# Kernel tuning notes

Hardware: AMD Instinct MI355X
Metric: run time of the kernel (lower is better)

## Reference

```python
import jax, jax.numpy as jnp
import numpy as np
import math

B, S, HID, H = 2, 4096, 512, 8
D_K = HID // H


def setup_inputs() -> dict:
    key = jax.random.key(0)
    ks = jax.random.split(key, 8)
    inp = {
        "query": jax.random.normal(ks[0], (B, S, HID), dtype=jnp.float32),
        "key": jax.random.normal(ks[1], (B, S, HID), dtype=jnp.float32),
        "value": jax.random.normal(ks[2], (B, S, HID), dtype=jnp.float32),
        "mask": jax.random.randint(ks[3], (B, S), 0, 2, dtype=jnp.int32),
        # conv1d kernel_size=1, bias=False -> plain [out,in] weights (xavier-normal-ish)
        "Wq": jax.random.normal(ks[4], (HID, HID), dtype=jnp.float32) * (1.0 / math.sqrt(HID)),
        "Wk": jax.random.normal(ks[5], (HID, HID), dtype=jnp.float32) * (1.0 / math.sqrt(HID)),
        "Wv": jax.random.normal(ks[6], (HID, HID), dtype=jnp.float32) * (1.0 / math.sqrt(HID)),
        "Wo": jax.random.normal(ks[7], (HID, HID), dtype=jnp.float32) * (1.0 / math.sqrt(HID)),
    }
    return inp


def reference(query, key, value, mask, Wq, Wk, Wv, Wo):
    b, s, _ = query.shape
    # conv1d(k=1, bias=False) projection == x @ W.T; split heads -> [b,h,s,d_k]
    def proj(x, W):
        return jnp.einsum('bsd,ed->bse', x, W).reshape(b, s, H, D_K).transpose(0, 2, 1, 3)
    q, k, v = proj(query, Wq), proj(key, Wk), proj(value, Wv)
    # NOTE: original scales by 1/log(d_k), not 1/sqrt(d_k)
    score = jnp.einsum('bhqd,bhkd->bhqk', q, k) / math.log(D_K)
    m = mask.reshape(b, 1, 1, s)  # broadcast over heads and query positions
    score = jnp.where(m == 0, jnp.float32(-1e30), score)
    attn = jax.nn.softmax(score, axis=-1)  # dropout is identity in eval
    x = jnp.einsum('bhqk,bhkd->bhqd', attn, v)
    x = x.transpose(0, 2, 1, 3).reshape(b, s, HID)
    return jnp.einsum('bsd,ed->bse', x, Wo)
```

## Files before the change

### kernel.cpp

```cpp
#include <hip/hip_runtime.h>
#include <hip/hip_bf16.h>
#include <cstdint>
#include <cstddef>


namespace {

constexpr int kB = 2, kS = 4096, kHid = 512, kH = 8, kDk = 64;
constexpr int kBH = kB * kH;
constexpr int kM = kB * kS;

typedef __attribute__((ext_vector_type(8))) short short8;
typedef __attribute__((ext_vector_type(4))) float floatx4;
typedef __attribute__((ext_vector_type(16))) float floatx16;
typedef __attribute__((ext_vector_type(4))) unsigned int uintx4;
typedef unsigned short u16;

__device__ __forceinline__ u16 bf16rne(float f) {
    uint32_t u = __float_as_uint(f);
    u += 0x7fffu + ((u >> 16) & 1u);
    return (u16)(u >> 16);
}
__device__ __forceinline__ uint32_t pk2(float lo, float hi) {
#if __has_builtin(__builtin_amdgcn_cvt_pk_bf16_f32)
    typedef __attribute__((ext_vector_type(2))) __bf16 bf2;
    bf2 h = __builtin_amdgcn_cvt_pk_bf16_f32(lo, hi);
    return __builtin_bit_cast(uint32_t, h);
#else
    return ((uint32_t)bf16rne(hi) << 16) | (uint32_t)bf16rne(lo);
#endif
}
__device__ __forceinline__ float fexp2(float x) {
#if __has_builtin(__builtin_amdgcn_exp2f)
    return __builtin_amdgcn_exp2f(x);
#else
    return exp2f(x);
#endif
}
__device__ __forceinline__ float bf2f(u16 v) {
    return __uint_as_float((uint32_t)v << 16);
}
__device__ __forceinline__ void plswap(uint32_t& a, uint32_t& b) {
#if __has_builtin(__builtin_amdgcn_permlane32_swap)
    typedef __attribute__((ext_vector_type(2))) unsigned int uint2v;
    uint2v r = __builtin_amdgcn_permlane32_swap(a, b, false, false);
    a = r[0]; b = r[1];
#else
    asm volatile("v_permlane32_swap_b32 %0, %1" : "+v"(a), "+v"(b));
#endif
}
__device__ __forceinline__ void gload16(const void* g, void* l) {
    __builtin_amdgcn_global_load_lds(
        (const __attribute__((address_space(1))) void*)g,
        (__attribute__((address_space(3))) void*)l, 16, 0, 0);
}

__global__ __launch_bounds__(256) void cvt_qw(const float* __restrict__ q,
    const float* __restrict__ k, const float* __restrict__ v,
    const float* __restrict__ w0, const float* __restrict__ w1,
    const float* __restrict__ w2, const float* __restrict__ w3,
    u16* __restrict__ xall, u16* __restrict__ wall) {
    const int bx = blockIdx.x;
    if (bx < 12288) {
        int z = bx >> 12;
        size_t i = (size_t)(bx & 4095) * 256 + threadIdx.x;
        const float* src = z == 0 ? q : (z == 1 ? k : v);
        float4 f = ((const float4*)src)[i];
        ushort4 o;
        o.x = bf16rne(f.x); o.y = bf16rne(f.y);
        o.z = bf16rne(f.z); o.w = bf16rne(f.w);
        ((ushort4*)(xall + (size_t)z * kM * kHid))[i] = o;
    } else {
        int r = bx - 12288;
        int z = r >> 8;
        size_t i = (size_t)(r & 255) * 256 + threadIdx.x;
        const float* src = z == 0 ? w0 : (z == 1 ? w1 : (z == 2 ? w2 : w3));
        float sc = (z == 0)
            ? (float)(1.4426950408889634 / (6.0 * 0.6931471805599453))
            : 1.0f;
        float4 f = ((const float4*)src)[i];
        ushort4 o;
        o.x = bf16rne(f.x * sc); o.y = bf16rne(f.y * sc);
        o.z = bf16rne(f.z * sc); o.w = bf16rne(f.w * sc);
        ((ushort4*)(wall + (size_t)z * kHid * kHid))[i] = o;
    }
}

__global__ __launch_bounds__(256) void cvt_mask(const int* __restrict__ mask,
    float* __restrict__ fb) {
    int i = blockIdx.x * 256 + threadIdx.x;
    fb[i] = mask[i] ? 0.0f : -1e30f;
}

__global__ __launch_bounds__(256, 3) void proj(const u16* __restrict__ xall,
    const u16* __restrict__ wall, u16* __restrict__ qp, u16* __restrict__ kp,
    u16* __restrict__ vt) {
    __shared__ float smt[4][16][68];
    const int z = blockIdx.z;
    const u16* x = xall + (size_t)z * kM * kHid;
    const u16* w = wall + (size_t)z * kHid * kHid;
    const int wv = threadIdx.x >> 6, lane = threadIdx.x & 63;
    const int quad = lane >> 4, l16 = lane & 15;
    const int mb = blockIdx.y * 128 + (wv >> 1) * 64;
    const int nb = blockIdx.x * 128 + (wv & 1) * 64;
    floatx4 acc[4][4] = {};
    const u16* xr = x + (size_t)(mb + l16) * kHid + quad * 8;
    const u16* wr = w + (size_t)(nb + l16) * kHid + quad * 8;
    for (int k0 = 0; k0 < kHid; k0 += 32) {
        short8 a[4], bt[4];
#pragma unroll
        for (int i = 0; i < 4; i++)
            a[i] = *(const short8*)(xr + (size_t)i * 16 * kHid + k0);
#pragma unroll
        for (int t = 0; t < 4; t++)
            bt[t] = *(const short8*)(wr + (size_t)t * 16 * kHid + k0);
#pragma unroll
        for (int i = 0; i < 4; i++)
#pragma unroll
        for (int t = 0; t < 4; t++)
            acc[i][t] = __builtin_amdgcn_mfma_f32_16x16x32_bf16(a[i], bt[t], acc[i][t], 0, 0, 0);
    }
    if (z < 2) {
        u16* dst = (z == 0) ? qp : kp;
        const int row16 = lane >> 2, cseg = (lane & 3) * 16;
#pragma unroll
        for (int i = 0; i < 4; i++) {
#pragma unroll
            for (int t = 0; t < 4; t++)
#pragma unroll
            for (int r = 0; r < 4; r++)
                smt[wv][quad * 4 + r][t * 16 + l16] = acc[i][t][r];
            __builtin_amdgcn_wave_barrier();
            const float* rp = &smt[wv][row16][cseg];
            float4 f0 = *(const float4*)(rp);
            float4 f1 = *(const float4*)(rp + 4);
            float4 f2 = *(const float4*)(rp + 8);
            float4 f3 = *(const float4*)(rp + 12);
            uint4 o0, o1;
            o0.x = pk2(f0.x, f0.y); o0.y = pk2(f0.z, f0.w);
            o0.z = pk2(f1.x, f1.y); o0.w = pk2(f1.z, f1.w);
            o1.x = pk2(f2.x, f2.y); o1.y = pk2(f2.z, f2.w);
            o1.z = pk2(f3.x, f3.y); o1.w = pk2(f3.z, f3.w);
            u16* dp = dst + (size_t)(mb + i * 16 + row16) * kHid + nb + cseg;
            *(uint4*)dp = o0;
            *(uint4*)(dp + 8) = o1;
            __builtin_amdgcn_wave_barrier();
        }
    } else {
#pragma unroll
        for (int i = 0; i < 4; i++)
#pragma unroll
        for (int t = 0; t < 4; t++) {
            int m0 = mb + i * 16 + quad * 4;
            int n = nb + t * 16 + l16;
            int b = m0 >> 12, s = m0 & (kS - 1);
            int h = n >> 6,   d = n & (kDk - 1);
            ushort4 o;
            o.x = bf16rne(acc[i][t][0]); o.y = bf16rne(acc[i][t][1]);
            o.z = bf16rne(acc[i][t][2]); o.w = bf16rne(acc[i][t][3]);
            *(ushort4*)(vt + ((size_t)(b * kH + h) * kDk + d) * kS + s) = o;
        }
    }
}

__global__ __launch_bounds__(256, 2) void attn(const u16* __restrict__ qp,
    const u16* __restrict__ kp, const u16* __restrict__ vt,
    const float* __restrict__ fbias, u16* __restrict__ ows,
    float* __restrict__ rsws) {
    union SmT {
        struct { u16 K[2][64][64]; u16 V[2][64][64]; } s;
        float ep[4][32][33];
    };
    __shared__ __align__(16) SmT sm;
    const int tid = threadIdx.x;
    const int wv = tid >> 6, l = tid & 63;
    const int hf = l >> 5, q32 = l & 31, l7 = l & 7;
    const int wg = blockIdx.x;
    const int bh = ((wg & 7) << 1) | ((wg >> 3) & 1);
    const int qb = (wg >> 4) & 15;
    const int kz = wg >> 8;
    const int b = bh >> 3, h = bh & 7;
    const int qbase = qb * 256 + wv * 64;
    const u16* Qb = qp + (size_t)b * kS * kHid + h * 64;
    const u16* Kb = kp + (size_t)b * kS * kHid + h * 64;
    const u16* Vb = vt + (size_t)bh * kDk * kS;
    const float* fm = fbias + b * kS;

    short8 qf[2][4];
#pragma unroll
    for (int qt = 0; qt < 2; qt++)
#pragma unroll
    for (int m = 0; m < 4; m++)
        qf[qt][m] = *(const short8*)(Qb + (size_t)(qbase + qt * 32 + q32) * kHid + m * 16 + hf * 8);

    floatx16 O[2][2] = {};
    float rs[2] = {0.0f, 0.0f};

    const int srow = l >> 3;
    const int pcol = (l7 ^ srow) * 8;
    const u16* pK = Kb + (size_t)(kz * 64 + wv * 8 + srow) * kHid + pcol;
    const u16* pV = Vb + (size_t)(wv * 8 + srow) * kS + kz * 64 + pcol;
    auto stage = [&](int ph) {
        gload16(pK,                        &sm.s.K[ph][wv * 8][0]);
        gload16(pK + (size_t)32 * kHid,    &sm.s.K[ph][wv * 8 + 32][0]);
        gload16(pV,                        &sm.s.V[ph][wv * 8][0]);
        gload16(pV + (size_t)32 * kS,      &sm.s.V[ph][wv * 8 + 32][0]);
        pK += (size_t)128 * kHid;
        pV += 128;
    };

    stage(0);
    __syncthreads();

    for (int s5 = 0; s5 < 32; ++s5) {
        const int ph = s5 & 1;
        const int kt = (kz + 2 * s5) * 64;
        if (s5 < 31) stage(ph ^ 1);
#pragma unroll
        for (int ks = 0; ks < 2; ++ks) {
            short8 kf[4];
#pragma unroll
            for (int m = 0; m < 4; m++)
                kf[m] = *(const short8*)&sm.s.K[ph][ks * 32 + q32][((2 * m + hf) ^ l7) * 8];
            short8 vf[2][2];
#pragma unroll
            for (int ds = 0; ds < 2; ds++)
#pragma unroll
            for (int tt = 0; tt < 2; tt++)
                vf[ds][tt] = *(const short8*)&sm.s.V[ph][ds * 32 + q32][((ks * 4 + tt * 2 + hf) ^ l7) * 8];
            const float* fp = fm + kt + ks * 32 + 4 * hf;
            float4 g0 = *(const float4*)(fp);
            float4 g1 = *(const float4*)(fp + 8);
            float4 g2 = *(const float4*)(fp + 16);
            float4 g3 = *(const float4*)(fp + 24);
#pragma unroll
            for (int qt = 0; qt < 2; ++qt) {
                floatx16 st;
                st[0] = g0.x;  st[1] = g0.y;  st[2] = g0.z;  st[3] = g0.w;
                st[4] = g1.x;  st[5] = g1.y;  st[6] = g1.z;  st[7] = g1.w;
                st[8] = g2.x;  st[9] = g2.y;  st[10] = g2.z; st[11] = g2.w;
                st[12] = g3.x; st[13] = g3.y; st[14] = g3.z; st[15] = g3.w;
#pragma unroll
                for (int m = 0; m < 4; m++)
                    st = __builtin_amdgcn_mfma_f32_32x32x16_bf16(kf[m], qf[qt][m], st, 0, 0, 0);
                float xx[16];
#pragma unroll
                for (int r = 0; r < 16; r++) xx[r] = fexp2(st[r]);
                rs[qt] += (((xx[0] + xx[1]) + (xx[2] + xx[3])) + ((xx[4] + xx[5]) + (xx[6] + xx[7])))
                        + (((xx[8] + xx[9]) + (xx[10] + xx[11])) + ((xx[12] + xx[13]) + (xx[14] + xx[15])));
                uint32_t w00 = pk2(xx[0], xx[1]),   w01 = pk2(xx[2], xx[3]);
                uint32_t w10 = pk2(xx[4], xx[5]),   w11 = pk2(xx[6], xx[7]);
                uint32_t w20 = pk2(xx[8], xx[9]),   w21 = pk2(xx[10], xx[11]);
                uint32_t w30 = pk2(xx[12], xx[13]), w31 = pk2(xx[14], xx[15]);
                plswap(w00, w10); plswap(w01, w11);
                plswap(w20, w30); plswap(w21, w31);
                uintx4 t0 = {w00, w01, w10, w11};
                uintx4 t1 = {w20, w21, w30, w31};
                short8 bf0 = __builtin_bit_cast(short8, t0);
                short8 bf1 = __builtin_bit_cast(short8, t1);
                O[qt][0] = __builtin_amdgcn_mfma_f32_32x32x16_bf16(vf[0][0], bf0, O[qt][0], 0, 0, 0);
                O[qt][0] = __builtin_amdgcn_mfma_f32_32x32x16_bf16(vf[0][1], bf1, O[qt][0], 0, 0, 0);
                O[qt][1] = __builtin_amdgcn_mfma_f32_32x32x16_bf16(vf[1][0], bf0, O[qt][1], 0, 0, 0);
                O[qt][1] = __builtin_amdgcn_mfma_f32_32x32x16_bf16(vf[1][1], bf1, O[qt][1], 0, 0, 0);
            }
        }
        __syncthreads();
    }

#pragma unroll
    for (int qt = 0; qt < 2; ++qt) {
        float r = rs[qt];
        r += __shfl_xor(r, 32);
        if (hf == 0)
            rsws[((size_t)kz * kBH + bh) * kS + qbase + qt * 32 + q32] = r;
        u16* Ob = ows + (((size_t)kz * kBH + bh) * kS + qbase + qt * 32) * kDk;
#pragma unroll
        for (int ds = 0; ds < 2; ds++) {
#pragma unroll
            for (int rr = 0; rr < 16; rr++)
                sm.ep[wv][q32][(rr & 3) + 8 * (rr >> 2) + 4 * hf] = O[qt][ds][rr];
            __builtin_amdgcn_wave_barrier();
            {
                const int qq = l >> 1, c0 = (l & 1) * 16;
                float f[16];
#pragma unroll
                for (int j = 0; j < 16; j++) f[j] = sm.ep[wv][qq][c0 + j];
                uint4 o0, o1;
                o0.x = pk2(f[0], f[1]);   o0.y = pk2(f[2], f[3]);
                o0.z = pk2(f[4], f[5]);   o0.w = pk2(f[6], f[7]);
                o1.x = pk2(f[8], f[9]);   o1.y = pk2(f[10], f[11]);
                o1.z = pk2(f[12], f[13]); o1.w = pk2(f[14], f[15]);
                u16* dp = Ob + (size_t)qq * kDk + ds * 32 + c0;
                *(uint4*)dp = o0;
                *(uint4*)(dp + 8) = o1;
            }
            __builtin_amdgcn_wave_barrier();
        }
    }
}

__global__ __launch_bounds__(256) void combine(const u16* __restrict__ ows,
    const float* __restrict__ rsws, u16* __restrict__ xo) {
    size_t i = (size_t)blockIdx.x * 256 + threadIdx.x;
    const int d8 = (int)(i & 7);
    const int s  = (int)((i >> 3) & (kS - 1));
    const int bh = (int)(i >> 15);
    const int b = bh >> 3, h = bh & 7;
    const size_t base = ((size_t)bh * kS + s) * kDk + d8 * 8;
    short8 a = *(const short8*)(ows + base);
    short8 c = *(const short8*)(ows + (size_t)kBH * kS * kDk + base);
    float r = rsws[(size_t)bh * kS + s] + rsws[(size_t)kBH * kS + (size_t)bh * kS + s];
    float inv = 1.0f / r;
    float e[8];
#pragma unroll
    for (int j = 0; j < 8; j++)
        e[j] = (bf2f((u16)a[j]) + bf2f((u16)c[j])) * inv;
    uint4 o;
    o.x = pk2(e[0], e[1]); o.y = pk2(e[2], e[3]);
    o.z = pk2(e[4], e[5]); o.w = pk2(e[6], e[7]);
    *(uint4*)(xo + ((size_t)b * kS + s) * kHid + h * 64 + d8 * 8) = o;
}

__global__ __launch_bounds__(256, 3) void oproj(const u16* __restrict__ x,
    const u16* __restrict__ w, float* __restrict__ out) {
    const int wv = threadIdx.x >> 6, lane = threadIdx.x & 63;
    const int quad = lane >> 4, l16 = lane & 15;
    const int mb = blockIdx.y * 128 + (wv >> 1) * 64;
    const int nb = blockIdx.x * 128 + (wv & 1) * 64;
    floatx4 acc[4][4] = {};
    const u16* xr = x + (size_t)(mb + l16) * kHid + quad * 8;
    const u16* wr = w + (size_t)(nb + l16) * kHid + quad * 8;
    for (int k0 = 0; k0 < kHid; k0 += 32) {
        short8 a[4], bt[4];
#pragma unroll
        for (int i = 0; i < 4; i++)
            a[i] = *(const short8*)(xr + (size_t)i * 16 * kHid + k0);
#pragma unroll
        for (int t = 0; t < 4; t++)
            bt[t] = *(const short8*)(wr + (size_t)t * 16 * kHid + k0);
#pragma unroll
        for (int i = 0; i < 4; i++)
#pragma unroll
        for (int t = 0; t < 4; t++)
            acc[i][t] = __builtin_amdgcn_mfma_f32_16x16x32_bf16(a[i], bt[t], acc[i][t], 0, 0, 0);
    }
#pragma unroll
    for (int i = 0; i < 4; i++)
#pragma unroll
    for (int t = 0; t < 4; t++)
#pragma unroll
    for (int r = 0; r < 4; r++) {
        int m = mb + i * 16 + quad * 4 + r;
        int n = nb + t * 16 + l16;
        out[(size_t)m * kHid + n] = acc[i][t][r];
    }
}

}

extern "C" void kernel_launch(void* const* d_in, const int* in_sizes, int n_in,
                              void* d_out, int out_size, void* d_ws, size_t ws_size,
                              hipStream_t stream) {
    const float* q  = (const float*)d_in[0];
    const float* k  = (const float*)d_in[1];
    const float* v  = (const float*)d_in[2];
    const int* mask = (const int*)d_in[3];
    const float* w0 = (const float*)d_in[4];
    const float* w1 = (const float*)d_in[5];
    const float* w2 = (const float*)d_in[6];
    const float* w3 = (const float*)d_in[7];
    float* out = (float*)d_out;

    u16* ws   = (u16*)d_ws;
    u16* xall = ws;
    u16* wall = xall + (size_t)3 * kM * kHid;
    u16* qp   = wall + (size_t)4 * kHid * kHid;
    u16* kp   = qp + (size_t)kBH * kS * kDk;
    u16* vt   = kp + (size_t)kBH * kS * kDk;
    u16* ows  = xall;
    float* fbias = (float*)(xall + (size_t)2 * kM * kHid);
    float* rsws  = fbias + (size_t)kB * kS;
    u16* xo   = qp;

    dim3 blk(256);
    cvt_qw <<<dim3(13312), blk, 0, stream>>>(q, k, v, w0, w1, w2, w3, xall, wall);
    proj   <<<dim3(kHid / 128, kM / 128, 3), blk, 0, stream>>>(xall, wall, qp, kp, vt);
    cvt_mask<<<dim3(kB * kS / 256), blk, 0, stream>>>(mask, fbias);
    attn   <<<dim3(512), blk, 0, stream>>>(qp, kp, vt, fbias, ows, rsws);
    combine<<<dim3(2048), blk, 0, stream>>>(ows, rsws, xo);
    oproj  <<<dim3(kHid / 128, kM / 128), blk, 0, stream>>>(
        xo, wall + (size_t)3 * kHid * kHid, out);
}
```

Baseline: 264.9 us.

## Split attention key range three ways and raise attn occupancy to three blocks

The attention kernel now splits the key sequence into three interleaved chunks instead of two. It launches 768 workgroups with a launch bound of three blocks per CU, and the combine kernel sums three partial outputs and row sums. To make room for the third partial buffer, the mask-bias and row-sum scratch move into the weight workspace region, which is dead by then. The row-sum reduction is also rewritten with packed float2 adds. The aim is more parallelism and better latency hiding. The cost is tighter register limits that could cause spills, plus extra partial-result traffic in combine.

```diff
diff --git a/kernel.cpp b/kernel.cpp
--- a/kernel.cpp
+++ b/kernel.cpp
@@ -9,8 +9,10 @@
 constexpr int kB = 2, kS = 4096, kHid = 512, kH = 8, kDk = 64;
 constexpr int kBH = kB * kH;
 constexpr int kM = kB * kS;
+constexpr int kKZ = 3;
 
 typedef __attribute__((ext_vector_type(8))) short short8;
+typedef __attribute__((ext_vector_type(2))) float float2v;
 typedef __attribute__((ext_vector_type(4))) float floatx4;
 typedef __attribute__((ext_vector_type(16))) float floatx16;
 typedef __attribute__((ext_vector_type(4))) unsigned int uintx4;
@@ -163,7 +165,7 @@
     }
 }
 
-__global__ __launch_bounds__(256, 2) void attn(const u16* __restrict__ qp,
+__global__ __launch_bounds__(256, 3) void attn(const u16* __restrict__ qp,
     const u16* __restrict__ kp, const u16* __restrict__ vt,
     const float* __restrict__ fbias, u16* __restrict__ ows,
     float* __restrict__ rsws) {
@@ -176,9 +178,13 @@
     const int wv = tid >> 6, l = tid & 63;
     const int hf = l >> 5, q32 = l & 31, l7 = l & 7;
     const int wg = blockIdx.x;
-    const int bh = ((wg & 7) << 1) | ((wg >> 3) & 1);
-    const int qb = (wg >> 4) & 15;
-    const int kz = wg >> 8;
+    const int xcd = wg & 7;
+    const int widx = wg >> 3;
+    const int bh = (xcd << 1) | (widx & 1);
+    const int rest = widx >> 1;
+    const int qb = rest & 15;
+    const int kz = rest >> 4;
+    const int nt = (kz == 0) ? 22 : 21;
     const int b = bh >> 3, h = bh & 7;
     const int qbase = qb * 256 + wv * 64;
     const u16* Qb = qp + (size_t)b * kS * kHid + h * 64;
@@ -205,17 +211,17 @@
         gload16(pK + (size_t)32 * kHid,    &sm.s.K[ph][wv * 8 + 32][0]);
         gload16(pV,                        &sm.s.V[ph][wv * 8][0]);
         gload16(pV + (size_t)32 * kS,      &sm.s.V[ph][wv * 8 + 32][0]);
-        pK += (size_t)128 * kHid;
-        pV += 128;
+        pK += (size_t)(kKZ * 64) * kHid;
+        pV += kKZ * 64;
     };
 
     stage(0);
     __syncthreads();
 
-    for (int s5 = 0; s5 < 32; ++s5) {
+    for (int s5 = 0; s5 < nt; ++s5) {
         const int ph = s5 & 1;
-        const int kt = (kz + 2 * s5) * 64;
-        if (s5 < 31) stage(ph ^ 1);
+        const int kt = (kz + kKZ * s5) * 64;
+        if (s5 < nt - 1) stage(ph ^ 1);
 #pragma unroll
         for (int ks = 0; ks < 2; ++ks) {
             short8 kf[4];
@@ -246,8 +252,14 @@
                 float xx[16];
 #pragma unroll
                 for (int r = 0; r < 16; r++) xx[r] = fexp2(st[r]);
-                rs[qt] += (((xx[0] + xx[1]) + (xx[2] + xx[3])) + ((xx[4] + xx[5]) + (xx[6] + xx[7])))
-                        + (((xx[8] + xx[9]) + (xx[10] + xx[11])) + ((xx[12] + xx[13]) + (xx[14] + xx[15])));
+                float2v a0 = {xx[0], xx[1]},  a1 = {xx[2], xx[3]};
+                float2v a2 = {xx[4], xx[5]},  a3 = {xx[6], xx[7]};
+                float2v a4 = {xx[8], xx[9]},  a5 = {xx[10], xx[11]};
+                float2v a6 = {xx[12], xx[13]}, a7 = {xx[14], xx[15]};
+                a0 += a1; a2 += a3; a4 += a5; a6 += a7;
+                a0 += a2; a4 += a6;
+                a0 += a4;
+                rs[qt] += a0[0] + a0[1];
                 uint32_t w00 = pk2(xx[0], xx[1]),   w01 = pk2(xx[2], xx[3]);
                 uint32_t w10 = pk2(xx[4], xx[5]),   w11 = pk2(xx[6], xx[7]);
                 uint32_t w20 = pk2(xx[8], xx[9]),   w21 = pk2(xx[10], xx[11]);
@@ -307,14 +319,18 @@
     const int bh = (int)(i >> 15);
     const int b = bh >> 3, h = bh & 7;
     const size_t base = ((size_t)bh * kS + s) * kDk + d8 * 8;
-    short8 a = *(const short8*)(ows + base);
-    short8 c = *(const short8*)(ows + (size_t)kBH * kS * kDk + base);
-    float r = rsws[(size_t)bh * kS + s] + rsws[(size_t)kBH * kS + (size_t)bh * kS + s];
+    const size_t kzs = (size_t)kBH * kS * kDk;
+    short8 a0 = *(const short8*)(ows + base);
+    short8 a1 = *(const short8*)(ows + kzs + base);
+    short8 a2 = *(const short8*)(ows + 2 * kzs + base);
+    float r = rsws[(size_t)bh * kS + s]
+            + rsws[(size_t)kBH * kS + (size_t)bh * kS + s]
+            + rsws[(size_t)2 * kBH * kS + (size_t)bh * kS + s];
     float inv = 1.0f / r;
     float e[8];
 #pragma unroll
     for (int j = 0; j < 8; j++)
-        e[j] = (bf2f((u16)a[j]) + bf2f((u16)c[j])) * inv;
+        e[j] = (bf2f((u16)a0[j]) + bf2f((u16)a1[j]) + bf2f((u16)a2[j])) * inv;
     uint4 o;
     o.x = pk2(e[0], e[1]); o.y = pk2(e[2], e[3]);
     o.z = pk2(e[4], e[5]); o.w = pk2(e[6], e[7]);
@@ -378,7 +394,7 @@
     u16* kp   = qp + (size_t)kBH * kS * kDk;
     u16* vt   = kp + (size_t)kBH * kS * kDk;
     u16* ows  = xall;
-    float* fbias = (float*)(xall + (size_t)2 * kM * kHid);
+    float* fbias = (float*)wall;
     float* rsws  = fbias + (size_t)kB * kS;
     u16* xo   = qp;
 
@@ -386,7 +402,7 @@
     cvt_qw <<<dim3(13312), blk, 0, stream>>>(q, k, v, w0, w1, w2, w3, xall, wall);
     proj   <<<dim3(kHid / 128, kM / 128, 3), blk, 0, stream>>>(xall, wall, qp, kp, vt);
     cvt_mask<<<dim3(kB * kS / 256), blk, 0, stream>>>(mask, fbias);
-    attn   <<<dim3(512), blk, 0, stream>>>(qp, kp, vt, fbias, ows, rsws);
+    attn   <<<dim3(768), blk, 0, stream>>>(qp, kp, vt, fbias, ows, rsws);
     combine<<<dim3(2048), blk, 0, stream>>>(ows, rsws, xo);
     oproj  <<<dim3(kHid / 128, kM / 128), blk, 0, stream>>>(
         xo, wall + (size_t)3 * kHid * kHid, out);
```

New measurement: 303.9 us. +14.8%, slower.

## Triple-buffer attention K/V/bias loads and fuse split-K combine into output projection

Applied to the files above, without the earlier changes.

The attention main loop moves from double to triple buffering. The mask bias is now staged into LDS alongside K and V through async global-to-LDS loads, and explicit vmcnt waits and barriers replace the per-iteration __syncthreads. The separate combine kernel is removed: oproj reads both split-K partial outputs and row sums, normalizes them, and builds its bf16 A fragments on the fly. This saves a launch and an intermediate round trip through memory, but the combine work is now repeated for every output column block. The row-sum reduction uses packed float2 adds, and fbias/rsws move into the dead weight workspace region.

```diff
diff --git a/kernel.cpp b/kernel.cpp
--- a/kernel.cpp
+++ b/kernel.cpp
@@ -11,6 +11,7 @@
 constexpr int kM = kB * kS;
 
 typedef __attribute__((ext_vector_type(8))) short short8;
+typedef __attribute__((ext_vector_type(2))) float float2v;
 typedef __attribute__((ext_vector_type(4))) float floatx4;
 typedef __attribute__((ext_vector_type(16))) float floatx16;
 typedef __attribute__((ext_vector_type(4))) unsigned int uintx4;
@@ -168,7 +169,7 @@
     const float* __restrict__ fbias, u16* __restrict__ ows,
     float* __restrict__ rsws) {
     union SmT {
-        struct { u16 K[2][64][64]; u16 V[2][64][64]; } s;
+        struct { u16 K[3][64][64]; u16 V[3][64][64]; float B[3][256]; } s;
         float ep[4][32][33];
     };
     __shared__ __align__(16) SmT sm;
@@ -200,39 +201,36 @@
     const int pcol = (l7 ^ srow) * 8;
     const u16* pK = Kb + (size_t)(kz * 64 + wv * 8 + srow) * kHid + pcol;
     const u16* pV = Vb + (size_t)(wv * 8 + srow) * kS + kz * 64 + pcol;
-    auto stage = [&](int ph) {
-        gload16(pK,                        &sm.s.K[ph][wv * 8][0]);
-        gload16(pK + (size_t)32 * kHid,    &sm.s.K[ph][wv * 8 + 32][0]);
-        gload16(pV,                        &sm.s.V[ph][wv * 8][0]);
-        gload16(pV + (size_t)32 * kS,      &sm.s.V[ph][wv * 8 + 32][0]);
+    const float* pB = fm + kz * 64 + (l & 15) * 4;
+    auto stage = [&](int buf) {
+        gload16(pK,                     &sm.s.K[buf][wv * 8][0]);
+        gload16(pK + (size_t)32 * kHid, &sm.s.K[buf][wv * 8 + 32][0]);
+        gload16(pV,                     &sm.s.V[buf][wv * 8][0]);
+        gload16(pV + (size_t)32 * kS,   &sm.s.V[buf][wv * 8 + 32][0]);
+        gload16(pB,                     &sm.s.B[buf][0]);
         pK += (size_t)128 * kHid;
         pV += 128;
+        pB += 128;
     };
 
-    stage(0);
-    __syncthreads();
-
-    for (int s5 = 0; s5 < 32; ++s5) {
-        const int ph = s5 & 1;
-        const int kt = (kz + 2 * s5) * 64;
-        if (s5 < 31) stage(ph ^ 1);
+    auto compute = [&](int buf) {
 #pragma unroll
         for (int ks = 0; ks < 2; ++ks) {
             short8 kf[4];
 #pragma unroll
             for (int m = 0; m < 4; m++)
-                kf[m] = *(const short8*)&sm.s.K[ph][ks * 32 + q32][((2 * m + hf) ^ l7) * 8];
+                kf[m] = *(const short8*)&sm.s.K[buf][ks * 32 + q32][((2 * m + hf) ^ l7) * 8];
             short8 vf[2][2];
 #pragma unroll
             for (int ds = 0; ds < 2; ds++)
 #pragma unroll
             for (int tt = 0; tt < 2; tt++)
-                vf[ds][tt] = *(const short8*)&sm.s.V[ph][ds * 32 + q32][((ks * 4 + tt * 2 + hf) ^ l7) * 8];
-            const float* fp = fm + kt + ks * 32 + 4 * hf;
-            float4 g0 = *(const float4*)(fp);
-            float4 g1 = *(const float4*)(fp + 8);
-            float4 g2 = *(const float4*)(fp + 16);
-            float4 g3 = *(const float4*)(fp + 24);
+                vf[ds][tt] = *(const short8*)&sm.s.V[buf][ds * 32 + q32][((ks * 4 + tt * 2 + hf) ^ l7) * 8];
+            const float* bb = &sm.s.B[buf][ks * 32 + 4 * hf];
+            float4 g0 = *(const float4*)(bb);
+            float4 g1 = *(const float4*)(bb + 8);
+            float4 g2 = *(const float4*)(bb + 16);
+            float4 g3 = *(const float4*)(bb + 24);
 #pragma unroll
             for (int qt = 0; qt < 2; ++qt) {
                 floatx16 st;
@@ -246,8 +244,14 @@
                 float xx[16];
 #pragma unroll
                 for (int r = 0; r < 16; r++) xx[r] = fexp2(st[r]);
-                rs[qt] += (((xx[0] + xx[1]) + (xx[2] + xx[3])) + ((xx[4] + xx[5]) + (xx[6] + xx[7])))
-                        + (((xx[8] + xx[9]) + (xx[10] + xx[11])) + ((xx[12] + xx[13]) + (xx[14] + xx[15])));
+                float2v a0 = {xx[0], xx[1]},  a1 = {xx[2], xx[3]};
+                float2v a2 = {xx[4], xx[5]},  a3 = {xx[6], xx[7]};
+                float2v a4 = {xx[8], xx[9]},  a5 = {xx[10], xx[11]};
+                float2v a6 = {xx[12], xx[13]}, a7 = {xx[14], xx[15]};
+                a0 += a1; a2 += a3; a4 += a5; a6 += a7;
+                a0 += a2; a4 += a6;
+                a0 += a4;
+                rs[qt] += a0[0] + a0[1];
                 uint32_t w00 = pk2(xx[0], xx[1]),   w01 = pk2(xx[2], xx[3]);
                 uint32_t w10 = pk2(xx[4], xx[5]),   w11 = pk2(xx[6], xx[7]);
                 uint32_t w20 = pk2(xx[8], xx[9]),   w21 = pk2(xx[10], xx[11]);
@@ -264,8 +268,26 @@
                 O[qt][1] = __builtin_amdgcn_mfma_f32_32x32x16_bf16(vf[1][1], bf1, O[qt][1], 0, 0, 0);
             }
         }
-        __syncthreads();
-    }
+    };
+
+    stage(0);
+    stage(1);
+    for (int t = 0; t < 30; ++t) {
+        asm volatile("s_waitcnt vmcnt(5)" ::: "memory");
+        __builtin_amdgcn_s_barrier();
+        __builtin_amdgcn_sched_barrier(0);
+        stage((t + 2) % 3);
+        compute(t % 3);
+    }
+    asm volatile("s_waitcnt vmcnt(5)" ::: "memory");
+    __builtin_amdgcn_s_barrier();
+    __builtin_amdgcn_sched_barrier(0);
+    compute(0);
+    asm volatile("s_waitcnt vmcnt(0)" ::: "memory");
+    __builtin_amdgcn_s_barrier();
+    __builtin_amdgcn_sched_barrier(0);
+    compute(1);
+    __syncthreads();
 
 #pragma unroll
     for (int qt = 0; qt < 2; ++qt) {
@@ -299,42 +321,38 @@
     }
 }
 
-__global__ __launch_bounds__(256) void combine(const u16* __restrict__ ows,
-    const float* __restrict__ rsws, u16* __restrict__ xo) {
-    size_t i = (size_t)blockIdx.x * 256 + threadIdx.x;
-    const int d8 = (int)(i & 7);
-    const int s  = (int)((i >> 3) & (kS - 1));
-    const int bh = (int)(i >> 15);
-    const int b = bh >> 3, h = bh & 7;
-    const size_t base = ((size_t)bh * kS + s) * kDk + d8 * 8;
-    short8 a = *(const short8*)(ows + base);
-    short8 c = *(const short8*)(ows + (size_t)kBH * kS * kDk + base);
-    float r = rsws[(size_t)bh * kS + s] + rsws[(size_t)kBH * kS + (size_t)bh * kS + s];
-    float inv = 1.0f / r;
-    float e[8];
-#pragma unroll
-    for (int j = 0; j < 8; j++)
-        e[j] = (bf2f((u16)a[j]) + bf2f((u16)c[j])) * inv;
-    uint4 o;
-    o.x = pk2(e[0], e[1]); o.y = pk2(e[2], e[3]);
-    o.z = pk2(e[4], e[5]); o.w = pk2(e[6], e[7]);
-    *(uint4*)(xo + ((size_t)b * kS + s) * kHid + h * 64 + d8 * 8) = o;
-}
-
-__global__ __launch_bounds__(256, 3) void oproj(const u16* __restrict__ x,
-    const u16* __restrict__ w, float* __restrict__ out) {
+__global__ __launch_bounds__(256, 3) void oproj(const u16* __restrict__ ows,
+    const float* __restrict__ rsws, const u16* __restrict__ w,
+    float* __restrict__ out) {
     const int wv = threadIdx.x >> 6, lane = threadIdx.x & 63;
     const int quad = lane >> 4, l16 = lane & 15;
     const int mb = blockIdx.y * 128 + (wv >> 1) * 64;
     const int nb = blockIdx.x * 128 + (wv & 1) * 64;
+    const size_t kzs = (size_t)kBH * kS * kDk;
     floatx4 acc[4][4] = {};
-    const u16* xr = x + (size_t)(mb + l16) * kHid + quad * 8;
     const u16* wr = w + (size_t)(nb + l16) * kHid + quad * 8;
     for (int k0 = 0; k0 < kHid; k0 += 32) {
+        const int h = (k0 + quad * 8) >> 6, d0 = (k0 + quad * 8) & (kDk - 1);
         short8 a[4], bt[4];
 #pragma unroll
-        for (int i = 0; i < 4; i++)
-            a[i] = *(const short8*)(xr + (size_t)i * 16 * kHid + k0);
+        for (int i = 0; i < 4; i++) {
+            const int m = mb + i * 16 + l16;
+            const int bb = m >> 12, ss = m & (kS - 1);
+            const int bh = bb * kH + h;
+            const size_t base = ((size_t)bh * kS + ss) * kDk + d0;
+            short8 p0 = *(const short8*)(ows + base);
+            short8 p1 = *(const short8*)(ows + kzs + base);
+            float r = rsws[(size_t)bh * kS + ss]
+                    + rsws[(size_t)kBH * kS + (size_t)bh * kS + ss];
+            float inv = 1.0f / r;
+            float e[8];
+#pragma unroll
+            for (int j = 0; j < 8; j++)
+                e[j] = (bf2f((u16)p0[j]) + bf2f((u16)p1[j])) * inv;
+            uintx4 u = {pk2(e[0], e[1]), pk2(e[2], e[3]),
+                        pk2(e[4], e[5]), pk2(e[6], e[7])};
+            a[i] = __builtin_bit_cast(short8, u);
+        }
 #pragma unroll
         for (int t = 0; t < 4; t++)
             bt[t] = *(const short8*)(wr + (size_t)t * 16 * kHid + k0);
@@ -378,16 +396,14 @@
     u16* kp   = qp + (size_t)kBH * kS * kDk;
     u16* vt   = kp + (size_t)kBH * kS * kDk;
     u16* ows  = xall;
-    float* fbias = (float*)(xall + (size_t)2 * kM * kHid);
+    float* fbias = (float*)wall;
     float* rsws  = fbias + (size_t)kB * kS;
-    u16* xo   = qp;
 
     dim3 blk(256);
     cvt_qw <<<dim3(13312), blk, 0, stream>>>(q, k, v, w0, w1, w2, w3, xall, wall);
     proj   <<<dim3(kHid / 128, kM / 128, 3), blk, 0, stream>>>(xall, wall, qp, kp, vt);
     cvt_mask<<<dim3(kB * kS / 256), blk, 0, stream>>>(mask, fbias);
     attn   <<<dim3(512), blk, 0, stream>>>(qp, kp, vt, fbias, ows, rsws);
-    combine<<<dim3(2048), blk, 0, stream>>>(ows, rsws, xo);
     oproj  <<<dim3(kHid / 128, kM / 128), blk, 0, stream>>>(
-        xo, wall + (size_t)3 * kHid * kHid, out);
-}
+        ows, rsws, wall + (size_t)3 * kHid * kHid, out);
+}
```

Result: slower. 279.7 us (+5.6%).
